# Optimization experiments

Measured on AMD Instinct MI355X. Metric: run time of the kernel, lower is better.

## Reference

```python
import jax, jax.numpy as jnp
import numpy as np

B, T, V, F = 32, 512, 64, 64
K_ORDER = 4


def setup_inputs() -> dict:
    key = jax.random.key(0)
    k1, k2, k3 = jax.random.split(key, 3)
    x = jax.random.normal(k1, (B, T, V, F), dtype=jnp.float32)
    W = jax.random.uniform(k2, (B, V, V), dtype=jnp.float32)
    # Keras 'uniform' initializer: U(-0.05, 0.05)
    Theta = jax.random.uniform(k3, (K_ORDER, F, F), dtype=jnp.float32, minval=-0.05, maxval=0.05)
    return {"x": x, "W": W, "Theta": Theta}


def _cheb_stack(W, k):
    """Faithful to the original: polynomial recurrence is ELEMENTWISE, not matmul."""
    b, v, _ = W.shape
    eye = jnp.eye(v, dtype=W.dtype)
    deg = W.sum(axis=1)                      # K.sum(W, axis=1) -> (B, V)
    L = deg[:, :, None] * eye - W            # D - W, (B, V, V)
    # lambda_max = 2.0 -> L_t = 2*L/2 - I = L - I
    L_t = L - eye
    polys = [jnp.broadcast_to(eye, (b, v, v)), L_t]
    for _ in range(2, k):
        polys.append(2.0 * L_t * polys[-1] - polys[-2])  # elementwise recurrence
    return jnp.stack(polys[:k], axis=0)      # (k, B, V, V)


def reference(x, W, Theta):
    k = Theta.shape[0]
    T_k = _cheb_stack(W, k)                                   # (k, B, V, V)
    # per timestep: sum_k (T_k^T @ x_t) @ theta_k, vectorized over t
    out = jnp.einsum('kbuv,btuf,kfg->btvg', T_k, x, Theta)    # (B, T, V, F)
    return jax.nn.relu(out) + jax.nn.sigmoid(x)
```

## Files before the change

kernel.cpp:

```cpp
#include <hip/hip_runtime.h>
#include <stdint.h>
#include <stddef.h>

#define Bn 32
#define Tn 512
#define Vn 64
#define Fn 64
#define TT 32

typedef __attribute__((ext_vector_type(8))) short bfx8;
typedef __attribute__((ext_vector_type(4))) float fx4;
typedef __attribute__((ext_vector_type(4))) int   ix4;
typedef __attribute__((ext_vector_type(2))) int   ix2;

__device__ __forceinline__ short f2bf(float f) {
    union { float f; uint32_t u; } c; c.f = f;
    uint32_t u = c.u;
    return (short)((u + 0x7FFFu + ((u >> 16) & 1u)) >> 16);
}
__device__ __forceinline__ int pkbf2(float a, float b) {
    uint32_t ua = __float_as_uint(a) + 0x8000u;
    uint32_t ub = __float_as_uint(b) + 0x8000u;
    return (int)__builtin_amdgcn_perm(ub, ua, 0x07060302u);
}

union Shmem {
    struct { float wt[64][65]; float ps[4][64]; float dg[64]; } s;
    short tf[32][64][8];
};

__global__ __launch_bounds__(256, 2) void gcjk_main(
    const float* __restrict__ x, const float* __restrict__ W,
    const float* __restrict__ Theta, float* __restrict__ out)
{
    __shared__ __align__(16) Shmem sm;
    __shared__ __align__(16) short xt[2][64 * 64];

    const int tid  = threadIdx.x;
    const int lane = tid & 63;
    const int wv   = tid >> 6;
    const int l15  = lane & 15;
    const int gg   = lane >> 4;
    const int sc = tid & 15, sa = tid >> 4;

    const int bid = blockIdx.x;
    const int b   = bid >> 4;
    const int t0  = (bid & 15) * TT;

    const float4* W4 = (const float4*)(W + b * (Vn * Vn));
    #pragma unroll
    for (int c = 0; c < 4; ++c) {
        float4 wq = W4[c * 256 + tid];
        int flat = (c * 256 + tid) * 4;
        int i = flat >> 6, j = flat & 63;
        sm.s.wt[i][j+0] = wq.x; sm.s.wt[i][j+1] = wq.y;
        sm.s.wt[i][j+2] = wq.z; sm.s.wt[i][j+3] = wq.w;
    }
    __syncthreads();

    {
        float s = 0.f;
        #pragma unroll
        for (int r = 0; r < 16; ++r) s += sm.s.wt[wv * 16 + r][lane];
        sm.s.ps[wv][lane] = s;
    }
    __syncthreads();
    if (tid < 64) sm.s.dg[tid] = sm.s.ps[0][tid] + sm.s.ps[1][tid] + sm.s.ps[2][tid] + sm.s.ps[3][tid];
    __syncthreads();

    bfx8 af[4][2];
    {
        const int v = 16 * wv + l15;
        #pragma unroll
        for (int s = 0; s < 2; ++s) {
            #pragma unroll
            for (int e = 0; e < 8; ++e) {
                int u = 32 * s + 8 * gg + e;
                float wuv = sm.s.wt[u][v];
                float lt  = ((u == v) ? (sm.s.dg[u] - 1.0f) : 0.0f) - wuv;
                float p0  = (u == v) ? 1.0f : 0.0f;
                float p1  = lt;
                float p2  = 2.0f * lt * p1 - p0;
                float p3  = 2.0f * lt * p2 - p1;
                af[0][s][e] = f2bf(p0);
                af[1][s][e] = f2bf(p1);
                af[2][s][e] = f2bf(p2);
                af[3][s][e] = f2bf(p3);
            }
        }
    }
    __syncthreads();

    #pragma unroll
    for (int fi = 0; fi < 8; ++fi) {
        int frag = wv * 8 + fi;
        int gt = frag >> 3, k = (frag >> 1) & 3, fh = frag & 1;
        int g  = 16 * gt + l15;
        #pragma unroll
        for (int e = 0; e < 8; ++e) {
            int f = 16 * (2 * fh + (e >> 2)) + 4 * gg + (e & 3);
            sm.tf[frag][lane][e] = f2bf(Theta[(k * Fn + f) * Fn + g]);
        }
    }

    const float* xs = x + (size_t)(b * Tn + t0) * (Vn * Fn);
    {
        fx4 xq[4];
        #pragma unroll
        for (int j = 0; j < 4; ++j) xq[j] = *(const fx4*)(xs + (4 * sa + j) * Fn + 4 * sc);
        #pragma unroll
        for (int r = 0; r < 4; ++r) {
            int f = 4 * sc + r;
            ix2 d; d[0] = pkbf2(xq[0][r], xq[1][r]); d[1] = pkbf2(xq[2][r], xq[3][r]);
            int g = sa ^ (f & 15);
            *(ix2*)&xt[0][f * 64 + g * 4] = d;
        }
    }
    __syncthreads();

    for (int ts = 0; ts < TT; ++ts) {
        const int cur = ts & 1;
        const float* xb = xs + (size_t)ts * (Vn * Fn);
        const int v = 16 * wv + l15;

        fx4 ex[4];
        #pragma unroll
        for (int gt = 0; gt < 4; ++gt)
            ex[gt] = *(const fx4*)(xb + v * Fn + 16 * gt + 4 * gg);

        fx4 xq[4];
        if (ts + 1 < TT) {
            const float* xn = xb + (Vn * Fn);
            #pragma unroll
            for (int j = 0; j < 4; ++j) xq[j] = *(const fx4*)(xn + (4 * sa + j) * Fn + 4 * sc);
        }

        const short* xcur = xt[cur];
        bfx8 xf[4][2];
        #pragma unroll
        for (int ft = 0; ft < 4; ++ft) {
            #pragma unroll
            for (int s = 0; s < 2; ++s) {
                int ub = 8 * s + 2 * gg;
                int g0 = ub ^ l15, g1 = (ub + 1) ^ l15;
                ix2 lo = *(const ix2*)&xcur[(16 * ft + l15) * 64 + g0 * 4];
                ix2 hi = *(const ix2*)&xcur[(16 * ft + l15) * 64 + g1 * 4];
                ix4 q; q[0] = lo[0]; q[1] = lo[1]; q[2] = hi[0]; q[3] = hi[1];
                xf[ft][s] = *(bfx8*)&q;
            }
        }

        fx4 oacc[4] = {fx4{0,0,0,0}, fx4{0,0,0,0}, fx4{0,0,0,0}, fx4{0,0,0,0}};
        #pragma unroll
        for (int k = 0; k < 4; ++k) {
            fx4 pacc[4] = {fx4{0,0,0,0}, fx4{0,0,0,0}, fx4{0,0,0,0}, fx4{0,0,0,0}};
            #pragma unroll
            for (int ft = 0; ft < 4; ++ft) {
                pacc[ft] = __builtin_amdgcn_mfma_f32_16x16x32_bf16(xf[ft][0], af[k][0], pacc[ft], 0, 0, 0);
                pacc[ft] = __builtin_amdgcn_mfma_f32_16x16x32_bf16(xf[ft][1], af[k][1], pacc[ft], 0, 0, 0);
            }
            #pragma unroll
            for (int fh = 0; fh < 2; ++fh) {
                fx4 pa = pacc[2*fh], pb = pacc[2*fh+1];
                ix4 pq;
                pq[0] = pkbf2(pa[0], pa[1]); pq[1] = pkbf2(pa[2], pa[3]);
                pq[2] = pkbf2(pb[0], pb[1]); pq[3] = pkbf2(pb[2], pb[3]);
                bfx8 pf = *(bfx8*)&pq;
                #pragma unroll
                for (int gt = 0; gt < 4; ++gt) {
                    bfx8 th = *(const bfx8*)&sm.tf[gt*8 + k*2 + fh][lane][0];
                    oacc[gt] = __builtin_amdgcn_mfma_f32_16x16x32_bf16(th, pf, oacc[gt], 0, 0, 0);
                }
            }
        }

        {
            float* ob = out + (size_t)(b * Tn + t0 + ts) * (Vn * Fn);
            #pragma unroll
            for (int gt = 0; gt < 4; ++gt) {
                fx4 xv = ex[gt];
                fx4 o  = oacc[gt];
                fx4 r;
                #pragma unroll
                for (int j = 0; j < 4; ++j)
                    r[j] = fmaxf(o[j], 0.f) + __builtin_amdgcn_rcpf(1.f + __expf(-xv[j]));
                *(fx4*)(ob + v * Fn + 16 * gt + 4 * gg) = r;
            }
        }

        if (ts + 1 < TT) {
            short* xnext = xt[cur ^ 1];
            #pragma unroll
            for (int r = 0; r < 4; ++r) {
                int f = 4 * sc + r;
                ix2 d; d[0] = pkbf2(xq[0][r], xq[1][r]); d[1] = pkbf2(xq[2][r], xq[3][r]);
                int g = sa ^ (f & 15);
                *(ix2*)&xt[cur ^ 1][f * 64 + g * 4] = d;
            }
            (void)xnext;
        }
        __syncthreads();
    }
}

extern "C" void kernel_launch(void* const* d_in, const int* in_sizes, int n_in,
                              void* d_out, int out_size, void* d_ws, size_t ws_size,
                              hipStream_t stream) {
    (void)in_sizes; (void)n_in; (void)out_size; (void)d_ws; (void)ws_size;
    const float* x  = (const float*)d_in[0];
    const float* W  = (const float*)d_in[1];
    const float* Th = (const float*)d_in[2];
    float* o = (float*)d_out;
    gcjk_main<<<dim3(Bn * (Tn / TT)), dim3(256), 0, stream>>>(x, W, Th, o);
}
```

Measured before the change: 119.7 us.

## Double block size to process two timesteps concurrently per iteration

Blocks grow from 256 to 512 threads, split into two groups of four waves. Each group handles alternating timesteps with its own double-buffered x tile, which halves the serial loop count and the number of block-wide barriers per timestep. The W load, degree reduction and Theta fragment setup are spread across all eight waves. Shared memory per block rises, and the launch bound of 512 threads with 4 blocks per SM may limit registers per thread.

```diff
diff --git a/kernel.cpp b/kernel.cpp
--- a/kernel.cpp
+++ b/kernel.cpp
@@ -7,6 +7,7 @@
 #define Vn 64
 #define Fn 64
 #define TT 32
+#define NI 16
 
 typedef __attribute__((ext_vector_type(8))) short bfx8;
 typedef __attribute__((ext_vector_type(4))) float fx4;
@@ -25,23 +26,26 @@
 }
 
 union Shmem {
-    struct { float wt[64][65]; float ps[4][64]; float dg[64]; } s;
+    struct { float wt[64][65]; float ps[8][64]; float dg[64]; } s;
     short tf[32][64][8];
 };
 
-__global__ __launch_bounds__(256, 2) void gcjk_main(
+__global__ __launch_bounds__(512, 4) void gcjk_main(
     const float* __restrict__ x, const float* __restrict__ W,
     const float* __restrict__ Theta, float* __restrict__ out)
 {
     __shared__ __align__(16) Shmem sm;
-    __shared__ __align__(16) short xt[2][64 * 64];
+    __shared__ __align__(16) short xt[2][2][64 * 64];
 
     const int tid  = threadIdx.x;
     const int lane = tid & 63;
-    const int wv   = tid >> 6;
+    const int wid  = tid >> 6;
+    const int wv   = wid & 3;
+    const int grp  = wid >> 2;
     const int l15  = lane & 15;
     const int gg   = lane >> 4;
-    const int sc = tid & 15, sa = tid >> 4;
+    const int gtid = tid & 255;
+    const int sc = gtid & 15, sa = gtid >> 4;
 
     const int bid = blockIdx.x;
     const int b   = bid >> 4;
@@ -49,9 +53,10 @@
 
     const float4* W4 = (const float4*)(W + b * (Vn * Vn));
     #pragma unroll
-    for (int c = 0; c < 4; ++c) {
-        float4 wq = W4[c * 256 + tid];
-        int flat = (c * 256 + tid) * 4;
+    for (int c = 0; c < 2; ++c) {
+        int idx = c * 512 + tid;
+        float4 wq = W4[idx];
+        int flat = idx * 4;
         int i = flat >> 6, j = flat & 63;
         sm.s.wt[i][j+0] = wq.x; sm.s.wt[i][j+1] = wq.y;
         sm.s.wt[i][j+2] = wq.z; sm.s.wt[i][j+3] = wq.w;
@@ -61,11 +66,16 @@
     {
         float s = 0.f;
         #pragma unroll
-        for (int r = 0; r < 16; ++r) s += sm.s.wt[wv * 16 + r][lane];
-        sm.s.ps[wv][lane] = s;
-    }
-    __syncthreads();
-    if (tid < 64) sm.s.dg[tid] = sm.s.ps[0][tid] + sm.s.ps[1][tid] + sm.s.ps[2][tid] + sm.s.ps[3][tid];
+        for (int r = 0; r < 8; ++r) s += sm.s.wt[wid * 8 + r][lane];
+        sm.s.ps[wid][lane] = s;
+    }
+    __syncthreads();
+    if (tid < 64) {
+        float s = 0.f;
+        #pragma unroll
+        for (int p = 0; p < 8; ++p) s += sm.s.ps[p][tid];
+        sm.s.dg[tid] = s;
+    }
     __syncthreads();
 
     bfx8 af[4][2];
@@ -92,8 +102,8 @@
     __syncthreads();
 
     #pragma unroll
-    for (int fi = 0; fi < 8; ++fi) {
-        int frag = wv * 8 + fi;
+    for (int fi = 0; fi < 4; ++fi) {
+        int frag = wid * 4 + fi;
         int gt = frag >> 3, k = (frag >> 1) & 3, fh = frag & 1;
         int g  = 16 * gt + l15;
         #pragma unroll
@@ -103,7 +113,7 @@
         }
     }
 
-    const float* xs = x + (size_t)(b * Tn + t0) * (Vn * Fn);
+    const float* xs = x + (size_t)(b * Tn + t0 + grp) * (Vn * Fn);
     {
         fx4 xq[4];
         #pragma unroll
@@ -113,15 +123,15 @@
             int f = 4 * sc + r;
             ix2 d; d[0] = pkbf2(xq[0][r], xq[1][r]); d[1] = pkbf2(xq[2][r], xq[3][r]);
             int g = sa ^ (f & 15);
-            *(ix2*)&xt[0][f * 64 + g * 4] = d;
-        }
-    }
-    __syncthreads();
-
-    for (int ts = 0; ts < TT; ++ts) {
-        const int cur = ts & 1;
-        const float* xb = xs + (size_t)ts * (Vn * Fn);
-        const int v = 16 * wv + l15;
+            *(ix2*)&xt[grp][0][f * 64 + g * 4] = d;
+        }
+    }
+    __syncthreads();
+
+    const int v = 16 * wv + l15;
+    for (int it = 0; it < NI; ++it) {
+        const int cur = it & 1;
+        const float* xb = xs + (size_t)(2 * it) * (Vn * Fn);
 
         fx4 ex[4];
         #pragma unroll
@@ -129,13 +139,13 @@
             ex[gt] = *(const fx4*)(xb + v * Fn + 16 * gt + 4 * gg);
 
         fx4 xq[4];
-        if (ts + 1 < TT) {
-            const float* xn = xb + (Vn * Fn);
+        if (it + 1 < NI) {
+            const float* xn = xb + 2 * (Vn * Fn);
             #pragma unroll
             for (int j = 0; j < 4; ++j) xq[j] = *(const fx4*)(xn + (4 * sa + j) * Fn + 4 * sc);
         }
 
-        const short* xcur = xt[cur];
+        const short* xcur = xt[grp][cur];
         bfx8 xf[4][2];
         #pragma unroll
         for (int ft = 0; ft < 4; ++ft) {
@@ -175,7 +185,7 @@
         }
 
         {
-            float* ob = out + (size_t)(b * Tn + t0 + ts) * (Vn * Fn);
+            float* ob = out + (size_t)(b * Tn + t0 + 2 * it + grp) * (Vn * Fn);
             #pragma unroll
             for (int gt = 0; gt < 4; ++gt) {
                 fx4 xv = ex[gt];
@@ -188,16 +198,14 @@
             }
         }
 
-        if (ts + 1 < TT) {
-            short* xnext = xt[cur ^ 1];
+        if (it + 1 < NI) {
             #pragma unroll
             for (int r = 0; r < 4; ++r) {
                 int f = 4 * sc + r;
                 ix2 d; d[0] = pkbf2(xq[0][r], xq[1][r]); d[1] = pkbf2(xq[2][r], xq[3][r]);
                 int g = sa ^ (f & 15);
-                *(ix2*)&xt[cur ^ 1][f * 64 + g * 4] = d;
-            }
-            (void)xnext;
+                *(ix2*)&xt[grp][cur ^ 1][f * 64 + g * 4] = d;
+            }
         }
         __syncthreads();
     }
@@ -211,5 +219,5 @@
     const float* W  = (const float*)d_in[1];
     const float* Th = (const float*)d_in[2];
     float* o = (float*)d_out;
-    gcjk_main<<<dim3(Bn * (Tn / TT)), dim3(256), 0, stream>>>(x, W, Th, o);
-}
+    gcjk_main<<<dim3(Bn * (Tn / TT)), dim3(512), 0, stream>>>(x, W, Th, o);
+}
```

Measured after the change: 135.5 us. +13.2%, slower.
